# Optimization experiments

Hardware: AMD Instinct MI355X
Metric: run time of the kernel (lower is better)

The kernel has to match this reference:

```python
import jax, jax.numpy as jnp
import numpy as np

N_MSB = 4      # bit planes
WB = 8         # weight quant bits
ABNM = 8       # activation quant bits (non-MVM)
NL = 0.1       # noise level


def quant(x, bits, r):
    # quant_pass: symmetric round-to-grid inside [-r, r]
    s = 2.0 ** (bits - 1)
    xs = jnp.clip(x / r, -1.0 + 1.0 / s, 1.0 - 1.0 / s)
    return jnp.round(xs * s) / s * r


def pact(x, a):
    # pact_a reduces to a hard clip to [-a, a]
    return jnp.clip(x, -a, a)


def bitsplit(x, n_msb):
    # x in [0,1] -> n_msb binary planes y[i] and beta weights l2/l1
    l1 = 2.0 ** n_msb - 1.0
    l2 = 2.0 ** (n_msb - 1 - jnp.arange(n_msb, dtype=x.dtype))  # [n_msb]
    y = jnp.floor(jnp.round(l1 * x)[None] / l2[:, None, None]) % 2.0  # [n_msb,B,D]
    return y, l2 / l1


def noisy_bmm(inp, W, b, key):
    # CustomMM_bmm.forward: quantized weights + additive gaussian noise
    kw, kb = jax.random.split(key)
    nw = jax.lax.stop_gradient(jax.random.normal(kw, W.shape, W.dtype) * W.max() * NL)
    nb = jax.lax.stop_gradient(jax.random.normal(kb, b.shape, b.dtype) * b.max() * NL)
    wq = quant(W, WB, 1.0)
    bq = quant(b, WB, 1.0)
    return jnp.einsum('mbi,mio->mbo', inp, wq + nw) + bq + nb  # [n_msb,B,4H]


def setup_inputs() -> dict:
    key = jax.random.key(0)
    ks = jax.random.split(key, 9)
    B, I, H, M = 4096, 256, 1024, N_MSB
    inp = {
        'input': jax.random.normal(ks[0], (B, I), jnp.float32),
        'hx': jax.random.normal(ks[1], (B, H), jnp.float32),
        'cx': jax.random.normal(ks[2], (B, H), jnp.float32),
        'weight_ih': jax.random.normal(ks[3], (M, I, 4 * H), jnp.float32),
        'weight_hh': jax.random.normal(ks[4], (M, H, 4 * H), jnp.float32),
        'bias_ih': jax.random.normal(ks[5], (M, 1, 4 * H), jnp.float32),
        'bias_hh': jax.random.normal(ks[6], (M, 1, 4 * H), jnp.float32),
        'a1': jnp.array([128.0], jnp.float32),
        'a3': jnp.array([1.0], jnp.float32),
        'a4': jnp.array([1.0], jnp.float32),
        'a5': jnp.array([1.0], jnp.float32),
        'a6': jnp.array([1.0], jnp.float32),
        'a7': jnp.array([4.0], jnp.float32),
        'a8': jnp.array([1.0], jnp.float32),
        'a9': jnp.array([4.0], jnp.float32),
        'a10': jnp.array([1.0], jnp.float32),
        'a11': jnp.array([4.0], jnp.float32),
    }
    return inp


def reference(input, hx, cx, weight_ih, weight_hh, bias_ih, bias_hh,
              a1, a3, a4, a5, a6, a7, a8, a9, a10, a11):
    k1, k2 = jax.random.split(jax.random.key(42))
    # input branch: clip -> map to [0,1] -> bit-split -> noisy bmm -> threshold -> beta-sum
    inp01 = (pact(input, a1) + a1) / (a1 * 2)
    y, beta = bitsplit(inp01, N_MSB)
    out = (noisy_bmm(y, weight_ih, bias_ih, k1) > 0.5).astype(input.dtype)
    part1 = (beta[:, None, None] * out).sum(0) * (a1 * 2) - a1
    # hidden branch (note: '+ a1' offset as in the original source)
    inp01 = (pact(hx, a11) + a1) / (a11 * 2)
    y, beta = bitsplit(inp01, N_MSB)
    out = (noisy_bmm(y, weight_hh, bias_hh, k2) > 0.5).astype(input.dtype)
    part2 = (beta[:, None, None] * out).sum(0) * (a11 * 2) - a11
    gates = part1 + part2  # [B, 4H]
    i, j, f, o = jnp.split(gates, 4, axis=1)
    fg = quant(pact(jax.nn.sigmoid(f), a3), ABNM, a3)
    ig = quant(pact(jax.nn.sigmoid(i), a4), ABNM, a4)
    act = quant(pact(jnp.tanh(j), a5), ABNM, a5)
    og = quant(pact(jax.nn.sigmoid(o), a6), ABNM, a6)
    gated_cell = quant(pact(cx * fg, a7), ABNM, a7)
    activated_input = quant(pact(ig * act, a8), ABNM, a8)
    new_c = quant(pact(gated_cell + activated_input, a9), ABNM, a9)
    activated_cell = quant(pact(jnp.tanh(new_c), a10), ABNM, a10)
    new_h = quant(pact(activated_cell * og, a11), ABNM, a11)
    return new_h, new_c
```

## Files before the change

### kernel.cpp

```cpp
#include <hip/hip_runtime.h>
#include <cstdint>
#include <cstddef>


typedef int v4i __attribute__((ext_vector_type(4)));

struct KPc { uint32_t a, b; };

__host__ __device__ constexpr KPc ctf(uint32_t k0, uint32_t k1v, uint32_t c0, uint32_t c1) {
  uint32_t ks2 = k0 ^ k1v ^ 0x1BD11BDAu;
  uint32_t x0 = c0 + k0;
  uint32_t x1 = c1 + k1v;
  uint32_t r0[4] = {13u, 15u, 26u, 6u};
  uint32_t r1[4] = {17u, 29u, 16u, 24u};
  uint32_t ks[3] = {k0, k1v, ks2};
  for (int g = 0; g < 5; ++g) {
    for (int j = 0; j < 4; ++j) {
      uint32_t rr = (g & 1) ? r1[j] : r0[j];
      x0 += x1;
      x1 = (x1 << rr) | (x1 >> (32u - rr));
      x1 ^= x0;
    }
    x0 += ks[(g + 1) % 3];
    x1 += ks[(g + 2) % 3] + (uint32_t)(g + 1);
  }
  return KPc{x0, x1};
}

constexpr KPc K1K  = ctf(0u, 42u, 0u, 0u);
constexpr KPc K2K  = ctf(0u, 42u, 0u, 1u);
constexpr KPc KWIH = ctf(K1K.a, K1K.b, 0u, 0u);
constexpr KPc KBIH = ctf(K1K.a, K1K.b, 0u, 1u);
constexpr KPc KWHH = ctf(K2K.a, K2K.b, 0u, 0u);
constexpr KPc KBHH = ctf(K2K.a, K2K.b, 0u, 1u);

__device__ __forceinline__ uint32_t tf_bits(uint32_t k0, uint32_t k1v, uint32_t j) {
  KPc r = ctf(k0, k1v, 0u, j);
  return r.a ^ r.b;
}

__device__ __forceinline__ unsigned encf(float f) {
  unsigned u = __float_as_uint(f);
  return (u & 0x80000000u) ? ~u : (u | 0x80000000u);
}
__device__ __forceinline__ float decf(unsigned e) {
  unsigned u = (e & 0x80000000u) ? (e & 0x7FFFFFFFu) : ~e;
  return __uint_as_float(u);
}

__global__ void rmax_kernel(const float* __restrict__ x, int n, unsigned* __restrict__ out) {
  unsigned best = 0u;
  for (int i = blockIdx.x * blockDim.x + threadIdx.x; i < n; i += gridDim.x * blockDim.x) {
    unsigned e = encf(x[i]);
    best = best > e ? best : e;
  }
  for (int off = 32; off > 0; off >>= 1) {
    unsigned o = __shfl_down(best, off, 64);
    best = best > o ? best : o;
  }
  __shared__ unsigned sm[4];
  int lane = threadIdx.x & 63, wv = threadIdx.x >> 6;
  if (lane == 0) sm[wv] = best;
  __syncthreads();
  if (threadIdx.x == 0) {
    unsigned b = sm[0];
    for (int i = 1; i < 4; ++i) b = b > sm[i] ? b : sm[i];
    atomicMax(out, b);
  }
}

__device__ __forceinline__ float xla_log1p(float t) {
  float small = __fmul_rn(__fadd_rn(__fmul_rn(-0.5f, t), 1.0f), t);
  float large = logf(__fadd_rn(t, 1.0f));
  return (fabsf(t) < 1e-4f) ? small : large;
}

__device__ __forceinline__ float xla_erfinv(float x) {
  float w = -xla_log1p(-__fmul_rn(x, x));
  float p;
  if (w < 5.0f) {
    float ww = __fadd_rn(w, -2.5f);
    p = 2.81022636e-08f;
    p = __fadd_rn(3.43273939e-07f, __fmul_rn(p, ww));
    p = __fadd_rn(-3.5233877e-06f, __fmul_rn(p, ww));
    p = __fadd_rn(-4.39150654e-06f, __fmul_rn(p, ww));
    p = __fadd_rn(0.00021858087f, __fmul_rn(p, ww));
    p = __fadd_rn(-0.00125372503f, __fmul_rn(p, ww));
    p = __fadd_rn(-0.00417768164f, __fmul_rn(p, ww));
    p = __fadd_rn(0.246640727f, __fmul_rn(p, ww));
    p = __fadd_rn(1.50140941f, __fmul_rn(p, ww));
  } else {
    float ww = __fadd_rn(sqrtf(w), -3.0f);
    p = -0.000200214257f;
    p = __fadd_rn(0.000100950558f, __fmul_rn(p, ww));
    p = __fadd_rn(0.00134934322f, __fmul_rn(p, ww));
    p = __fadd_rn(-0.00367342844f, __fmul_rn(p, ww));
    p = __fadd_rn(0.00573950773f, __fmul_rn(p, ww));
    p = __fadd_rn(-0.0076224613f, __fmul_rn(p, ww));
    p = __fadd_rn(0.00943887047f, __fmul_rn(p, ww));
    p = __fadd_rn(1.00167406f, __fmul_rn(p, ww));
    p = __fadd_rn(2.83297682f, __fmul_rn(p, ww));
  }
  return __fmul_rn(p, x);
}

__device__ __forceinline__ float normal_from_bits(uint32_t bits) {
  float u01 = __uint_as_float((bits >> 9) | 0x3f800000u) - 1.0f;
  const float lo = -0x1.fffffep-1f;
  float u = fmaxf(lo, __fadd_rn(__fmul_rn(u01, 2.0f), lo));
  return __fmul_rn(0x1.6a09e6p+0f, xla_erfinv(u));
}

__device__ __forceinline__ float quantw(float x) {
  float xs = fminf(fmaxf(x, -0.9921875f), 0.9921875f);
  return __fmul_rn(rintf(__fmul_rn(xs, 128.0f)), 0.0078125f);
}

__global__ void gen_t0_kernel(const float* __restrict__ W, float* __restrict__ T0,
                              const unsigned* __restrict__ encp) {
  int j = blockIdx.x * 256 + threadIdx.x;
  if (j >= 1048576) return;
  float wmax = decf(*encp);
  float nrm = normal_from_bits(tf_bits(KWIH.a, KWIH.b, (uint32_t)j));
  float nw = __fmul_rn(__fmul_rn(nrm, wmax), 0.1f);
  T0[j] = __fadd_rn(quantw(W[j]), nw);
}

__global__ void gen_bias_kernel(const float* __restrict__ bsrc, float* __restrict__ bq,
                                float* __restrict__ nb, int n,
                                const unsigned* __restrict__ encp, uint32_t k0, uint32_t k1v) {
  int j = blockIdx.x * 256 + threadIdx.x;
  if (j >= n) return;
  float bmax = decf(*encp);
  float nrm = normal_from_bits(tf_bits(k0, k1v, (uint32_t)j));
  bq[j] = quantw(bsrc[j]);
  nb[j] = __fmul_rn(__fmul_rn(nrm, bmax), 0.1f);
}

__global__ __launch_bounds__(256) void kv_kernel(
    const float* __restrict__ x, const float* __restrict__ ap,
    const float* __restrict__ offp, unsigned char* __restrict__ kvT, int Kdim) {
  __shared__ unsigned char tile[64][65];
  const int tid = threadIdx.x;
  const int bt = blockIdx.x * 64, it = blockIdx.y * 64;
  const float a = ap[0], off = offp[0];
#pragma unroll
  for (int e = 0; e < 16; ++e) {
    int idx = e * 256 + tid;
    int bl = idx >> 6, il = idx & 63;
    float v = fmaxf(-a, fminf(x[(size_t)(bt + bl) * Kdim + it + il], a));
    float t = __fdiv_rn(__fadd_rn(v, off), __fmul_rn(a, 2.0f));
    int k = (int)rintf(__fmul_rn(15.0f, t));
    tile[il][bl] = (unsigned char)(k & 15);
  }
  __syncthreads();
#pragma unroll
  for (int e = 0; e < 16; ++e) {
    int idx = e * 256 + tid;
    int il = idx >> 6, bl = idx & 63;
    kvT[(size_t)(it + il) * 4096 + bt + bl] = tile[il][bl];
  }
}

__global__ void gen_ahh_kernel(const float* __restrict__ hx, const float* __restrict__ a11p,
                               const float* __restrict__ a1p, signed char* __restrict__ A) {
  int j = blockIdx.x * 256 + threadIdx.x;
  if (j >= 4096 * 1024) return;
  float a = a11p[0], off = a1p[0];
  float v = fmaxf(-a, fminf(hx[j], a));
  float t = __fdiv_rn(__fadd_rn(v, off), __fmul_rn(a, 2.0f));
  int kq = (int)rintf(__fmul_rn(15.0f, t));
  A[j]                      = (signed char)((kq >> 3) & 1);
  A[(size_t)(1 << 22) + j]  = (signed char)((kq >> 2) & 1);
  A[(size_t)(2 << 22) + j]  = (signed char)((kq >> 1) & 1);
  A[(size_t)(3 << 22) + j]  = (signed char)(kq & 1);
}

__global__ void gen_aih_kernel(const float* __restrict__ input, const float* __restrict__ a1p,
                               signed char* __restrict__ A) {
  int j = blockIdx.x * 256 + threadIdx.x;
  if (j >= 4096 * 256) return;
  float a = a1p[0];
  float v = fmaxf(-a, fminf(input[j], a));
  float t = __fdiv_rn(__fadd_rn(v, a), __fmul_rn(a, 2.0f));
  int kq = (int)rintf(__fmul_rn(15.0f, t));
  A[j]                  = (signed char)((kq >> 2) & 1);
  A[1048576 + j]        = (signed char)((kq >> 1) & 1);
  A[2097152 + j]        = (signed char)(kq & 1);
}

__global__ __launch_bounds__(256) void gen_bt_kernel(
    const float* __restrict__ W, signed char* __restrict__ Bt,
    const unsigned* __restrict__ encp, int K, int m0, int nPlanes,
    uint32_t k0k, uint32_t k1k) {
  __shared__ signed char lhi[64 * 68];
  __shared__ signed char llo[64 * 68];
  const int tid = threadIdx.x;
  const int m = m0 + blockIdx.z;
  const int kt = blockIdx.y * 64, ct = blockIdx.x * 64;
  const float wmax = decf(*encp);
#pragma unroll 4
  for (int i = 0; i < 16; ++i) {
    int e = i * 256 + tid;
    int kl = e >> 6, cl = e & 63;
    uint32_t j = (uint32_t)(((m * K + kt + kl) << 12) + ct + cl);
    float nrm = normal_from_bits(tf_bits(k0k, k1k, j));
    float t = __fadd_rn(quantw(W[j]), __fmul_rn(__fmul_rn(nrm, wmax), 0.1f));
    int ti = (int)rintf(__fmul_rn(t, 6144.0f));
    int hi = (ti + 128) >> 8;
    int lo = ti - (hi << 8);
    lhi[cl * 68 + kl] = (signed char)hi;
    llo[cl * 68 + kl] = (signed char)lo;
  }
  __syncthreads();
  const size_t planeElems = (size_t)K << 12;
  signed char* bh = Bt + (size_t)blockIdx.z * planeElems;
  signed char* bl = Bt + (size_t)(nPlanes + blockIdx.z) * planeElems;
#pragma unroll 4
  for (int i = 0; i < 16; ++i) {
    int f = i * 256 + tid;
    int cl = f >> 6, kl = f & 63;
    size_t o = (size_t)(ct + cl) * K + kt + kl;
    bh[o] = lhi[cl * 68 + kl];
    bl[o] = llo[cl * 68 + kl];
  }
}

__global__ __launch_bounds__(256) void gemm_p0_kernel(
    const float* __restrict__ T0, const float* __restrict__ bq, const float* __restrict__ nb,
    const unsigned char* __restrict__ kvT, unsigned char* __restrict__ Kp) {
  const int tid = threadIdx.x, lane = tid & 63, wv = tid >> 6;
  const int c0 = blockIdx.x * 32;
  const int row = blockIdx.y * 256 + wv * 64 + lane;

  float acc[32];
#pragma unroll
  for (int j = 0; j < 32; ++j) acc[j] = 0.0f;

  const unsigned char* kvp = kvT + row;
#pragma unroll 2
  for (int k = 0; k < 256; ++k) {
    unsigned nib = kvp[(size_t)k << 12];
    float f = (float)((nib >> 3) & 1u);
    const float4* tp = (const float4*)(T0 + ((size_t)k << 12) + c0);
    float4 tv[8];
#pragma unroll
    for (int q = 0; q < 8; ++q) tv[q] = tp[q];
#pragma unroll
    for (int q = 0; q < 8; ++q) {
      acc[q * 4 + 0] = __builtin_fmaf(f, tv[q].x, acc[q * 4 + 0]);
      acc[q * 4 + 1] = __builtin_fmaf(f, tv[q].y, acc[q * 4 + 1]);
      acc[q * 4 + 2] = __builtin_fmaf(f, tv[q].z, acc[q * 4 + 2]);
      acc[q * 4 + 3] = __builtin_fmaf(f, tv[q].w, acc[q * 4 + 3]);
    }
  }

#pragma unroll
  for (int j = 0; j < 32; ++j) {
    int col = c0 + j;
    float s = __fadd_rn(__fadd_rn(acc[j], bq[col]), nb[col]);
    Kp[((size_t)row << 12) + col] = (s > 0.5f) ? (unsigned char)8 : (unsigned char)0;
  }
}

typedef __attribute__((address_space(3))) signed char lds_i8;
typedef __attribute__((address_space(1))) const signed char g_i8;

__device__ __forceinline__ void glds16(const signed char* g, signed char* l) {
  __builtin_amdgcn_global_load_lds((g_i8*)g, (lds_i8*)l, 16, 0, 0);
}

__global__ __launch_bounds__(256, 3) void gemm_mfma_kernel(
    const signed char* __restrict__ Ahh, const signed char* __restrict__ Bthh,
    const signed char* __restrict__ Aih, const signed char* __restrict__ Btih,
    const float* __restrict__ bqh, const float* __restrict__ nbh,
    const float* __restrict__ bqi, const float* __restrict__ nbi,
    unsigned char* __restrict__ Kp) {
  const int tid = threadIdx.x;
  const int lane = tid & 63, wv = tid >> 6;
  const int col0 = blockIdx.x * 64;
  const int row0 = blockIdx.y * 128;
  const int wrow = (wv >> 1) * 64;
  const int wcol = (wv & 1) * 32;

  __shared__ __align__(16) signed char smbuf[3][16384];
  const int HOFF = 8192, LOFF = 12288;

  const int l15 = lane & 15;
  const int cc  = (((lane >> 4) ^ ((lane >> 1) & 3)) << 4);
  const int xq  = ((((lane & 3) ^ ((lane >> 3) & 3))) << 4);
  const int lr  = lane >> 2;

  uint32_t k12[4][2];
#pragma unroll
  for (int rf = 0; rf < 4; ++rf) { k12[rf][0] = 0u; k12[rf][1] = 0u; }

  for (int sub = 0; sub < 7; ++sub) {
    int K, w;
    const signed char *A, *Bh, *Bl;
    const float *bqp, *nbp;
    if (sub < 4) {
      int m = sub;
      K = 1024;
      A  = Ahh  + ((size_t)m << 22);
      Bh = Bthh + ((size_t)m << 22);
      Bl = Bthh + ((size_t)(4 + m) << 22);
      bqp = bqh + (m << 12); nbp = nbh + (m << 12);
      w = (1 << (3 - m)) << 4;
    } else {
      int m = sub - 3;
      K = 256;
      A  = Aih  + ((size_t)(m - 1) << 20);
      Bh = Btih + ((size_t)(m - 1) << 20);
      Bl = Btih + ((size_t)(3 + m - 1) << 20);
      bqp = bqi + (m << 12); nbp = nbi + (m << 12);
      w = 1 << (3 - m);
    }

    const size_t soff = (size_t)lr * K + xq;
    const signed char* gA  = A  + (size_t)(row0 + 32 * wv) * K + soff;
    const signed char* gA2 = gA + (size_t)16 * K;
    const signed char* gH  = Bh + (size_t)(col0 + 16 * wv) * K + soff;
    const signed char* gL  = Bl + (size_t)(col0 + 16 * wv) * K + soff;

    auto stage = [&](signed char* base, int k0) {
      glds16(gA  + k0, base + (32 * wv) * 64);
      glds16(gA2 + k0, base + (32 * wv + 16) * 64);
      glds16(gH  + k0, base + HOFF + (16 * wv) * 64);
      glds16(gL  + k0, base + LOFF + (16 * wv) * 64);
    };

    v4i ach[4][2], acl[4][2];
    v4i zero = {0, 0, 0, 0};
#pragma unroll
    for (int rf = 0; rf < 4; ++rf)
#pragma unroll
      for (int cf = 0; cf < 2; ++cf) { ach[rf][cf] = zero; acl[rf][cf] = zero; }

    signed char* bc = &smbuf[0][0];
    signed char* bn = &smbuf[1][0];
    signed char* bf = &smbuf[2][0];

    const int nt = K >> 6;
    stage(bc, 0);
    stage(bn, 64);

    for (int t = 0; t < nt; ++t) {
      if (t + 1 < nt) {
        asm volatile("s_waitcnt vmcnt(4)" ::: "memory");
      } else {
        asm volatile("s_waitcnt vmcnt(0)" ::: "memory");
      }
      __builtin_amdgcn_s_barrier();
      __builtin_amdgcn_sched_barrier(0);
      if (t + 2 < nt) stage(bf, (t + 2) << 6);

      v4i af[4], bfh[2], bfl[2];
#pragma unroll
      for (int rf = 0; rf < 4; ++rf)
        af[rf] = *(const v4i*)(bc + (wrow + rf * 16 + l15) * 64 + cc);
#pragma unroll
      for (int cf = 0; cf < 2; ++cf) {
        bfh[cf] = *(const v4i*)(bc + HOFF + (wcol + cf * 16 + l15) * 64 + cc);
        bfl[cf] = *(const v4i*)(bc + LOFF + (wcol + cf * 16 + l15) * 64 + cc);
      }
#pragma unroll
      for (int rf = 0; rf < 4; ++rf)
#pragma unroll
        for (int cf = 0; cf < 2; ++cf) {
          ach[rf][cf] = __builtin_amdgcn_mfma_i32_16x16x64_i8(af[rf], bfh[cf], ach[rf][cf], 0, 0, 0);
          acl[rf][cf] = __builtin_amdgcn_mfma_i32_16x16x64_i8(af[rf], bfl[cf], acl[rf][cf], 0, 0, 0);
        }
      signed char* tmp = bc; bc = bn; bn = bf; bf = tmp;
    }
    __syncthreads();

#pragma unroll
    for (int cf = 0; cf < 2; ++cf) {
      int col = col0 + wcol + cf * 16 + l15;
      float bqc = bqp[col];
      float nbc = nbp[col];
#pragma unroll
      for (int rf = 0; rf < 4; ++rf)
#pragma unroll
        for (int r = 0; r < 4; ++r) {
          int tot = ach[rf][cf][r] * 256 + acl[rf][cf][r];
          float s = __fmul_rn((float)tot, (1.0f / 6144.0f));
          float s2 = __fadd_rn(__fadd_rn(s, bqc), nbc);
          if (s2 > 0.5f) k12[rf][cf] += ((uint32_t)w << (8 * r));
        }
    }
  }

#pragma unroll
  for (int rf = 0; rf < 4; ++rf)
#pragma unroll
    for (int cf = 0; cf < 2; ++cf)
#pragma unroll
      for (int r = 0; r < 4; ++r) {
        int row = row0 + wrow + rf * 16 + ((lane >> 4) << 2) + r;
        int col = col0 + wcol + cf * 16 + l15;
        size_t o = ((size_t)row << 12) + col;
        Kp[o] = (unsigned char)(Kp[o] | ((k12[rf][cf] >> (8 * r)) & 255u));
      }
}

__device__ __forceinline__ float quant8(float x, float r) {
  float xs = __fdiv_rn(x, r);
  xs = fminf(fmaxf(xs, -0.9921875f), 0.9921875f);
  float q = rintf(__fmul_rn(xs, 128.0f));
  return __fmul_rn(__fdiv_rn(q, 128.0f), r);
}
__device__ __forceinline__ float pactf(float x, float a) { return fminf(fmaxf(x, -a), a); }
__device__ __forceinline__ double sigd(double x) { return 1.0 / (1.0 + exp(-x)); }

__global__ void tail_kernel(const unsigned char* __restrict__ Kp, const float* __restrict__ cx,
                            const float* a1p, const float* a3p, const float* a4p,
                            const float* a5p, const float* a6p, const float* a7p,
                            const float* a8p, const float* a9p, const float* a10p,
                            const float* a11p, float* __restrict__ out) {
  int idx = blockIdx.x * 256 + threadIdx.x;
  if (idx >= 4096 * 1024) return;
  int b = idx >> 10, h = idx & 1023;
  double a1 = (double)a1p[0], a11 = (double)a11p[0];
  const unsigned char* row = Kp + (size_t)b * 4096 + h;
  int pI = row[0], pJ = row[1024], pF = row[2048], pO = row[3072];
  auto gate = [&](int pk) -> double {
    double s1 = (double)(pk & 15) * (1.0 / 15.0);
    double s2 = (double)(pk >> 4) * (1.0 / 15.0);
    return (s1 * (2.0 * a1) - a1) + (s2 * (2.0 * a11) - a11);
  };
  double gi = gate(pI), gj = gate(pJ), gf = gate(pF), go = gate(pO);
  float a3 = a3p[0], a4 = a4p[0], a5 = a5p[0], a6 = a6p[0];
  float a7 = a7p[0], a8 = a8p[0], a9 = a9p[0], a10 = a10p[0], a11f = a11p[0];
  float fg  = quant8(pactf((float)sigd(gf), a3), a3);
  float ig  = quant8(pactf((float)sigd(gi), a4), a4);
  float act = quant8(pactf((float)tanh(gj), a5), a5);
  float og  = quant8(pactf((float)sigd(go), a6), a6);
  float cxv = cx[idx];
  float gc  = quant8(pactf(__fmul_rn(cxv, fg), a7), a7);
  float ai  = quant8(pactf(__fmul_rn(ig, act), a8), a8);
  float nc  = quant8(pactf(__fadd_rn(gc, ai), a9), a9);
  float ac  = quant8(pactf((float)tanh((double)nc), a10), a10);
  float nh  = quant8(pactf(__fmul_rn(ac, og), a11f), a11f);
  out[idx] = nh;
  out[4194304 + idx] = nc;
}

extern "C" void kernel_launch(void* const* d_in, const int* in_sizes, int n_in,
                              void* d_out, int out_size, void* d_ws, size_t ws_size,
                              hipStream_t stream) {
  const float* input = (const float*)d_in[0];
  const float* hx    = (const float*)d_in[1];
  const float* cx    = (const float*)d_in[2];
  const float* wih   = (const float*)d_in[3];
  const float* whh   = (const float*)d_in[4];
  const float* bih   = (const float*)d_in[5];
  const float* bhh   = (const float*)d_in[6];
  const float* a1p   = (const float*)d_in[7];
  const float* a3p   = (const float*)d_in[8];
  const float* a4p   = (const float*)d_in[9];
  const float* a5p   = (const float*)d_in[10];
  const float* a6p   = (const float*)d_in[11];
  const float* a7p   = (const float*)d_in[12];
  const float* a8p   = (const float*)d_in[13];
  const float* a9p   = (const float*)d_in[14];
  const float* a10p  = (const float*)d_in[15];
  const float* a11p  = (const float*)d_in[16];

  char* ws = (char*)d_ws;
  unsigned* enc        = (unsigned*)ws;
  float* T0            = (float*)(ws + 256);
  float* bq_ih         = (float*)(ws + 256 + 4194304);
  float* nb_ih         = bq_ih + 16384;
  float* bq_hh         = nb_ih + 16384;
  float* nb_hh         = bq_hh + 16384;
  unsigned char* kv_ih = (unsigned char*)(nb_hh + 16384);
  signed char* A_hh    = (signed char*)(kv_ih + 1048576);
  signed char* Bt_hh   = A_hh + 16777216;
  signed char* A_ih    = Bt_hh + 33554432;
  signed char* Bt_ih   = A_ih + 3145728;
  unsigned char* Kp    = (unsigned char*)(Bt_ih + 6291456);

  hipMemsetAsync(enc, 0, 64, stream);
  rmax_kernel<<<512, 256, 0, stream>>>(wih, 4 * 256 * 4096, enc + 0);
  rmax_kernel<<<512, 256, 0, stream>>>(whh, 4 * 1024 * 4096, enc + 1);
  rmax_kernel<<<64, 256, 0, stream>>>(bih, 16384, enc + 2);
  rmax_kernel<<<64, 256, 0, stream>>>(bhh, 16384, enc + 3);

  kv_kernel<<<dim3(64, 4), 256, 0, stream>>>(input, a1p, a1p, kv_ih, 256);
  gen_aih_kernel<<<4096, 256, 0, stream>>>(input, a1p, A_ih);
  gen_ahh_kernel<<<16384, 256, 0, stream>>>(hx, a11p, a1p, A_hh);

  gen_bias_kernel<<<64, 256, 0, stream>>>(bih, bq_ih, nb_ih, 16384, enc + 2, KBIH.a, KBIH.b);
  gen_bias_kernel<<<64, 256, 0, stream>>>(bhh, bq_hh, nb_hh, 16384, enc + 3, KBHH.a, KBHH.b);

  gen_t0_kernel<<<4096, 256, 0, stream>>>(wih, T0, enc + 0);
  gen_bt_kernel<<<dim3(64, 16, 4), 256, 0, stream>>>(whh, Bt_hh, enc + 1, 1024, 0, 4,
                                                     KWHH.a, KWHH.b);
  gen_bt_kernel<<<dim3(64, 4, 3), 256, 0, stream>>>(wih, Bt_ih, enc + 0, 256, 1, 3,
                                                    KWIH.a, KWIH.b);

  gemm_p0_kernel<<<dim3(128, 16), 256, 0, stream>>>(T0, bq_ih, nb_ih, kv_ih, Kp);
  gemm_mfma_kernel<<<dim3(64, 32), 256, 0, stream>>>(A_hh, Bt_hh, A_ih, Bt_ih,
                                                     bq_hh, nb_hh, bq_ih, nb_ih, Kp);

  tail_kernel<<<16384, 256, 0, stream>>>(Kp, cx, a1p, a3p, a4p, a5p, a6p, a7p, a8p, a9p,
                                         a10p, a11p, (float*)d_out);
}
```

Measured before the change: 673.6 us.

## Load MFMA B fragments straight to registers and stage p0 T0 in LDS

In the int8 MFMA GEMM, the high and low B-plane fragments are no longer staged through LDS. Each lane loads its 16-byte fragment directly from global memory into registers, one k-tile ahead. This halves the LDS triple-buffer, which now holds only A, and removes the B LDS writes and reads, with the loop unrolled by two to ping-pong the register buffers. Separately, the p0 kernel first copies its 256x32 T0 tile into shared memory so the inner loop reads LDS instead of repeatedly reading global memory. The risks are less coalesced direct global loads for B, extra register pressure, and 32KB of LDS use in p0.

Result: slower. 866.8 us (+28.7%).

```diff
diff --git a/kernel.cpp b/kernel.cpp
--- a/kernel.cpp
+++ b/kernel.cpp
@@ -229,9 +229,17 @@
 __global__ __launch_bounds__(256) void gemm_p0_kernel(
     const float* __restrict__ T0, const float* __restrict__ bq, const float* __restrict__ nb,
     const unsigned char* __restrict__ kvT, unsigned char* __restrict__ Kp) {
+  __shared__ __align__(16) float lt[256 * 32];
   const int tid = threadIdx.x, lane = tid & 63, wv = tid >> 6;
   const int c0 = blockIdx.x * 32;
   const int row = blockIdx.y * 256 + wv * 64 + lane;
+
+#pragma unroll
+  for (int e = 0; e < 32; ++e) {
+    int idx = e * 256 + tid;
+    lt[idx] = T0[((size_t)(idx >> 5) << 12) + c0 + (idx & 31)];
+  }
+  __syncthreads();
 
   float acc[32];
 #pragma unroll
@@ -242,7 +250,7 @@
   for (int k = 0; k < 256; ++k) {
     unsigned nib = kvp[(size_t)k << 12];
     float f = (float)((nib >> 3) & 1u);
-    const float4* tp = (const float4*)(T0 + ((size_t)k << 12) + c0);
+    const float4* tp = (const float4*)(lt + (k << 5));
     float4 tv[8];
 #pragma unroll
     for (int q = 0; q < 8; ++q) tv[q] = tp[q];
@@ -283,13 +291,13 @@
   const int wrow = (wv >> 1) * 64;
   const int wcol = (wv & 1) * 32;
 
-  __shared__ __align__(16) signed char smbuf[3][16384];
-  const int HOFF = 8192, LOFF = 12288;
+  __shared__ __align__(16) signed char smbuf[3][8192];
 
   const int l15 = lane & 15;
   const int cc  = (((lane >> 4) ^ ((lane >> 1) & 3)) << 4);
   const int xq  = ((((lane & 3) ^ ((lane >> 3) & 3))) << 4);
   const int lr  = lane >> 2;
+  const int kch = (lane >> 4) << 4;
 
   uint32_t k12[4][2];
 #pragma unroll
@@ -320,14 +328,12 @@
     const size_t soff = (size_t)lr * K + xq;
     const signed char* gA  = A  + (size_t)(row0 + 32 * wv) * K + soff;
     const signed char* gA2 = gA + (size_t)16 * K;
-    const signed char* gH  = Bh + (size_t)(col0 + 16 * wv) * K + soff;
-    const signed char* gL  = Bl + (size_t)(col0 + 16 * wv) * K + soff;
-
-    auto stage = [&](signed char* base, int k0) {
+    const signed char* pBh = Bh + (size_t)(col0 + wcol + l15) * K + kch;
+    const signed char* pBl = Bl + (size_t)(col0 + wcol + l15) * K + kch;
+
+    auto stageA = [&](signed char* base, int k0) {
       glds16(gA  + k0, base + (32 * wv) * 64);
       glds16(gA2 + k0, base + (32 * wv + 16) * 64);
-      glds16(gH  + k0, base + HOFF + (16 * wv) * 64);
-      glds16(gL  + k0, base + LOFF + (16 * wv) * 64);
     };
 
     v4i ach[4][2], acl[4][2];
@@ -342,36 +348,56 @@
     signed char* bf = &smbuf[2][0];
 
     const int nt = K >> 6;
-    stage(bc, 0);
-    stage(bn, 64);
-
-    for (int t = 0; t < nt; ++t) {
+
+    v4i b0h[2], b0l[2], b1h[2], b1l[2];
+
+    stageA(bc, 0);
+    __builtin_amdgcn_sched_barrier(0);
+#pragma unroll
+    for (int cf = 0; cf < 2; ++cf) {
+      b0h[cf] = *(const v4i*)(pBh + (size_t)cf * 16 * K);
+      b0l[cf] = *(const v4i*)(pBl + (size_t)cf * 16 * K);
+    }
+    __builtin_amdgcn_sched_barrier(0);
+    stageA(bn, 64);
+
+    auto body = [&](int t, v4i (&uh)[2], v4i (&ul)[2], v4i (&lh)[2], v4i (&ll)[2]) {
       if (t + 1 < nt) {
-        asm volatile("s_waitcnt vmcnt(4)" ::: "memory");
+        asm volatile("s_waitcnt vmcnt(2)" ::: "memory");
       } else {
         asm volatile("s_waitcnt vmcnt(0)" ::: "memory");
       }
       __builtin_amdgcn_s_barrier();
       __builtin_amdgcn_sched_barrier(0);
-      if (t + 2 < nt) stage(bf, (t + 2) << 6);
-
-      v4i af[4], bfh[2], bfl[2];
+      if (t + 1 < nt) {
+        int k0 = (t + 1) << 6;
+#pragma unroll
+        for (int cf = 0; cf < 2; ++cf) {
+          lh[cf] = *(const v4i*)(pBh + (size_t)cf * 16 * K + k0);
+          ll[cf] = *(const v4i*)(pBl + (size_t)cf * 16 * K + k0);
+        }
+      }
+      __builtin_amdgcn_sched_barrier(0);
+      if (t + 2 < nt) stageA(bf, (t + 2) << 6);
+      __builtin_amdgcn_sched_barrier(0);
+
+      v4i af[4];
 #pragma unroll
       for (int rf = 0; rf < 4; ++rf)
         af[rf] = *(const v4i*)(bc + (wrow + rf * 16 + l15) * 64 + cc);
 #pragma unroll
-      for (int cf = 0; cf < 2; ++cf) {
-        bfh[cf] = *(const v4i*)(bc + HOFF + (wcol + cf * 16 + l15) * 64 + cc);
-        bfl[cf] = *(const v4i*)(bc + LOFF + (wcol + cf * 16 + l15) * 64 + cc);
-      }
-#pragma unroll
       for (int rf = 0; rf < 4; ++rf)
 #pragma unroll
         for (int cf = 0; cf < 2; ++cf) {
-          ach[rf][cf] = __builtin_amdgcn_mfma_i32_16x16x64_i8(af[rf], bfh[cf], ach[rf][cf], 0, 0, 0);
-          acl[rf][cf] = __builtin_amdgcn_mfma_i32_16x16x64_i8(af[rf], bfl[cf], acl[rf][cf], 0, 0, 0);
+          ach[rf][cf] = __builtin_amdgcn_mfma_i32_16x16x64_i8(af[rf], uh[cf], ach[rf][cf], 0, 0, 0);
+          acl[rf][cf] = __builtin_amdgcn_mfma_i32_16x16x64_i8(af[rf], ul[cf], acl[rf][cf], 0, 0, 0);
         }
       signed char* tmp = bc; bc = bn; bn = bf; bf = tmp;
+    };
+
+    for (int t = 0; t < nt; t += 2) {
+      body(t,     b0h, b0l, b1h, b1l);
+      body(t + 1, b1h, b1l, b0h, b0l);
     }
     __syncthreads();
 
```

## Merge prep launches into two kernels and use lookup tables in tail

Applied to the files above, without the earlier changes.

The four max-reduction launches become a single kernel, and the nine input and weight preparation launches become one large kernel that picks its sub-task from the block index. The tail kernel now builds small shared-memory lookup tables for the gate activations (the inputs are 8-bit codes) and for tanh of the quantized cell. This removes the per-element double-precision exp and tanh, and uses a grid-stride loop with fewer blocks. The aim is to cut launch overhead and tail compute. The cost is divergent branching inside the merged prep kernel and a table-setup step in every tail block.

Result: faster. 582.1 us (-13.6%).

```diff
diff --git a/kernel.cpp b/kernel.cpp
--- a/kernel.cpp
+++ b/kernel.cpp
@@ -48,9 +48,10 @@
   return __uint_as_float(u);
 }
 
-__global__ void rmax_kernel(const float* __restrict__ x, int n, unsigned* __restrict__ out) {
+__device__ __forceinline__ void rmax_seg(const float* __restrict__ x, int n,
+                                         unsigned* __restrict__ out, int rbid, int nblk) {
   unsigned best = 0u;
-  for (int i = blockIdx.x * blockDim.x + threadIdx.x; i < n; i += gridDim.x * blockDim.x) {
+  for (int i = rbid * 256 + threadIdx.x; i < n; i += nblk * 256) {
     unsigned e = encf(x[i]);
     best = best > e ? best : e;
   }
@@ -67,6 +68,16 @@
     for (int i = 1; i < 4; ++i) b = b > sm[i] ? b : sm[i];
     atomicMax(out, b);
   }
+}
+
+__global__ void rmax_all_kernel(const float* __restrict__ wih, const float* __restrict__ whh,
+                                const float* __restrict__ bih, const float* __restrict__ bhh,
+                                unsigned* __restrict__ enc) {
+  int b = blockIdx.x;
+  if (b < 512)       rmax_seg(wih, 4 * 256 * 4096,  enc + 0, b,        512);
+  else if (b < 1024) rmax_seg(whh, 4 * 1024 * 4096, enc + 1, b - 512,  512);
+  else if (b < 1088) rmax_seg(bih, 16384,           enc + 2, b - 1024, 64);
+  else               rmax_seg(bhh, 16384,           enc + 3, b - 1088, 64);
 }
 
 __device__ __forceinline__ float xla_log1p(float t) {
@@ -116,33 +127,12 @@
   return __fmul_rn(rintf(__fmul_rn(xs, 128.0f)), 0.0078125f);
 }
 
-__global__ void gen_t0_kernel(const float* __restrict__ W, float* __restrict__ T0,
-                              const unsigned* __restrict__ encp) {
-  int j = blockIdx.x * 256 + threadIdx.x;
-  if (j >= 1048576) return;
-  float wmax = decf(*encp);
-  float nrm = normal_from_bits(tf_bits(KWIH.a, KWIH.b, (uint32_t)j));
-  float nw = __fmul_rn(__fmul_rn(nrm, wmax), 0.1f);
-  T0[j] = __fadd_rn(quantw(W[j]), nw);
-}
-
-__global__ void gen_bias_kernel(const float* __restrict__ bsrc, float* __restrict__ bq,
-                                float* __restrict__ nb, int n,
-                                const unsigned* __restrict__ encp, uint32_t k0, uint32_t k1v) {
-  int j = blockIdx.x * 256 + threadIdx.x;
-  if (j >= n) return;
-  float bmax = decf(*encp);
-  float nrm = normal_from_bits(tf_bits(k0, k1v, (uint32_t)j));
-  bq[j] = quantw(bsrc[j]);
-  nb[j] = __fmul_rn(__fmul_rn(nrm, bmax), 0.1f);
-}
-
-__global__ __launch_bounds__(256) void kv_kernel(
-    const float* __restrict__ x, const float* __restrict__ ap,
-    const float* __restrict__ offp, unsigned char* __restrict__ kvT, int Kdim) {
-  __shared__ unsigned char tile[64][65];
+__device__ void do_kv(const float* __restrict__ x, const float* __restrict__ ap,
+                      const float* __restrict__ offp, unsigned char* __restrict__ kvT,
+                      int Kdim, int bx, int by, unsigned char* sh) {
+  unsigned char (*tile)[65] = (unsigned char (*)[65])sh;
   const int tid = threadIdx.x;
-  const int bt = blockIdx.x * 64, it = blockIdx.y * 64;
+  const int bt = bx * 64, it = by * 64;
   const float a = ap[0], off = offp[0];
 #pragma unroll
   for (int e = 0; e < 16; ++e) {
@@ -162,9 +152,22 @@
   }
 }
 
-__global__ void gen_ahh_kernel(const float* __restrict__ hx, const float* __restrict__ a11p,
-                               const float* __restrict__ a1p, signed char* __restrict__ A) {
-  int j = blockIdx.x * 256 + threadIdx.x;
+__device__ void do_aih(const float* __restrict__ input, const float* __restrict__ a1p,
+                       signed char* __restrict__ A, int rbid) {
+  int j = rbid * 256 + threadIdx.x;
+  if (j >= 4096 * 256) return;
+  float a = a1p[0];
+  float v = fmaxf(-a, fminf(input[j], a));
+  float t = __fdiv_rn(__fadd_rn(v, a), __fmul_rn(a, 2.0f));
+  int kq = (int)rintf(__fmul_rn(15.0f, t));
+  A[j]                  = (signed char)((kq >> 2) & 1);
+  A[1048576 + j]        = (signed char)((kq >> 1) & 1);
+  A[2097152 + j]        = (signed char)(kq & 1);
+}
+
+__device__ void do_ahh(const float* __restrict__ hx, const float* __restrict__ a11p,
+                       const float* __restrict__ a1p, signed char* __restrict__ A, int rbid) {
+  int j = rbid * 256 + threadIdx.x;
   if (j >= 4096 * 1024) return;
   float a = a11p[0], off = a1p[0];
   float v = fmaxf(-a, fminf(hx[j], a));
@@ -176,28 +179,36 @@
   A[(size_t)(3 << 22) + j]  = (signed char)(kq & 1);
 }
 
-__global__ void gen_aih_kernel(const float* __restrict__ input, const float* __restrict__ a1p,
-                               signed char* __restrict__ A) {
-  int j = blockIdx.x * 256 + threadIdx.x;
-  if (j >= 4096 * 256) return;
-  float a = a1p[0];
-  float v = fmaxf(-a, fminf(input[j], a));
-  float t = __fdiv_rn(__fadd_rn(v, a), __fmul_rn(a, 2.0f));
-  int kq = (int)rintf(__fmul_rn(15.0f, t));
-  A[j]                  = (signed char)((kq >> 2) & 1);
-  A[1048576 + j]        = (signed char)((kq >> 1) & 1);
-  A[2097152 + j]        = (signed char)(kq & 1);
-}
-
-__global__ __launch_bounds__(256) void gen_bt_kernel(
-    const float* __restrict__ W, signed char* __restrict__ Bt,
-    const unsigned* __restrict__ encp, int K, int m0, int nPlanes,
-    uint32_t k0k, uint32_t k1k) {
-  __shared__ signed char lhi[64 * 68];
-  __shared__ signed char llo[64 * 68];
+__device__ void do_bias(const float* __restrict__ bsrc, float* __restrict__ bq,
+                        float* __restrict__ nb, int n, const unsigned* __restrict__ encp,
+                        uint32_t k0, uint32_t k1v, int rbid) {
+  int j = rbid * 256 + threadIdx.x;
+  if (j >= n) return;
+  float bmax = decf(*encp);
+  float nrm = normal_from_bits(tf_bits(k0, k1v, (uint32_t)j));
+  bq[j] = quantw(bsrc[j]);
+  nb[j] = __fmul_rn(__fmul_rn(nrm, bmax), 0.1f);
+}
+
+__device__ void do_t0(const float* __restrict__ W, float* __restrict__ T0,
+                      const unsigned* __restrict__ encp, int rbid) {
+  int j = rbid * 256 + threadIdx.x;
+  if (j >= 1048576) return;
+  float wmax = decf(*encp);
+  float nrm = normal_from_bits(tf_bits(KWIH.a, KWIH.b, (uint32_t)j));
+  float nw = __fmul_rn(__fmul_rn(nrm, wmax), 0.1f);
+  T0[j] = __fadd_rn(quantw(W[j]), nw);
+}
+
+__device__ void do_bt(const float* __restrict__ W, signed char* __restrict__ Bt,
+                      const unsigned* __restrict__ encp, int K, int m0, int nPlanes,
+                      uint32_t k0k, uint32_t k1k, int bx, int by, int bz,
+                      unsigned char* sh) {
+  signed char* lhi = (signed char*)sh;
+  signed char* llo = (signed char*)sh + 4352;
   const int tid = threadIdx.x;
-  const int m = m0 + blockIdx.z;
-  const int kt = blockIdx.y * 64, ct = blockIdx.x * 64;
+  const int m = m0 + bz;
+  const int kt = by * 64, ct = bx * 64;
   const float wmax = decf(*encp);
 #pragma unroll 4
   for (int i = 0; i < 16; ++i) {
@@ -214,8 +225,8 @@
   }
   __syncthreads();
   const size_t planeElems = (size_t)K << 12;
-  signed char* bh = Bt + (size_t)blockIdx.z * planeElems;
-  signed char* bl = Bt + (size_t)(nPlanes + blockIdx.z) * planeElems;
+  signed char* bh = Bt + (size_t)bz * planeElems;
+  signed char* bl = Bt + (size_t)(nPlanes + bz) * planeElems;
 #pragma unroll 4
   for (int i = 0; i < 16; ++i) {
     int f = i * 256 + tid;
@@ -223,6 +234,39 @@
     size_t o = (size_t)(ct + cl) * K + kt + kl;
     bh[o] = lhi[cl * 68 + kl];
     bl[o] = llo[cl * 68 + kl];
+  }
+}
+
+__global__ __launch_bounds__(256) void prep_all_kernel(
+    const float* __restrict__ input, const float* __restrict__ hx,
+    const float* __restrict__ wih, const float* __restrict__ whh,
+    const float* __restrict__ bih, const float* __restrict__ bhh,
+    const float* __restrict__ a1p, const float* __restrict__ a11p,
+    const unsigned* __restrict__ enc,
+    unsigned char* __restrict__ kvT, signed char* __restrict__ A_ih,
+    signed char* __restrict__ A_hh, float* __restrict__ bq_ih, float* __restrict__ nb_ih,
+    float* __restrict__ bq_hh, float* __restrict__ nb_hh, float* __restrict__ T0,
+    signed char* __restrict__ Bt_hh, signed char* __restrict__ Bt_ih) {
+  __shared__ __align__(16) unsigned char sh[8704];
+  int b = blockIdx.x;
+  if (b < 256) {
+    do_kv(input, a1p, a1p, kvT, 256, b & 63, b >> 6, sh);
+  } else if (b < 4352) {
+    do_aih(input, a1p, A_ih, b - 256);
+  } else if (b < 20736) {
+    do_ahh(hx, a11p, a1p, A_hh, b - 4352);
+  } else if (b < 20800) {
+    do_bias(bih, bq_ih, nb_ih, 16384, enc + 2, KBIH.a, KBIH.b, b - 20736);
+  } else if (b < 20864) {
+    do_bias(bhh, bq_hh, nb_hh, 16384, enc + 3, KBHH.a, KBHH.b, b - 20800);
+  } else if (b < 24960) {
+    do_t0(wih, T0, enc + 0, b - 20864);
+  } else if (b < 29056) {
+    int t = b - 24960;
+    do_bt(whh, Bt_hh, enc + 1, 1024, 0, 4, KWHH.a, KWHH.b, t & 63, (t >> 6) & 15, t >> 10, sh);
+  } else {
+    int t = b - 29056;
+    do_bt(wih, Bt_ih, enc + 0, 256, 1, 3, KWIH.a, KWIH.b, t & 63, (t >> 6) & 3, t >> 8, sh);
   }
 }
 
@@ -414,37 +458,55 @@
 __device__ __forceinline__ float pactf(float x, float a) { return fminf(fmaxf(x, -a), a); }
 __device__ __forceinline__ double sigd(double x) { return 1.0 / (1.0 + exp(-x)); }
 
-__global__ void tail_kernel(const unsigned char* __restrict__ Kp, const float* __restrict__ cx,
-                            const float* a1p, const float* a3p, const float* a4p,
-                            const float* a5p, const float* a6p, const float* a7p,
-                            const float* a8p, const float* a9p, const float* a10p,
-                            const float* a11p, float* __restrict__ out) {
-  int idx = blockIdx.x * 256 + threadIdx.x;
-  if (idx >= 4096 * 1024) return;
-  int b = idx >> 10, h = idx & 1023;
-  double a1 = (double)a1p[0], a11 = (double)a11p[0];
-  const unsigned char* row = Kp + (size_t)b * 4096 + h;
-  int pI = row[0], pJ = row[1024], pF = row[2048], pO = row[3072];
-  auto gate = [&](int pk) -> double {
+__global__ __launch_bounds__(256) void tail_kernel(
+    const unsigned char* __restrict__ Kp, const float* __restrict__ cx,
+    const float* a1p, const float* a3p, const float* a4p,
+    const float* a5p, const float* a6p, const float* a7p,
+    const float* a8p, const float* a9p, const float* a10p,
+    const float* a11p, float* __restrict__ out) {
+  __shared__ float Tf[256], Ti[256], Tj[256], To[256], Tac[256];
+  const int tid = threadIdx.x;
+  const double a1 = (double)a1p[0], a11 = (double)a11p[0];
+  const float a3 = a3p[0], a4 = a4p[0], a5 = a5p[0], a6 = a6p[0];
+  const float a7 = a7p[0], a8 = a8p[0], a9 = a9p[0], a10 = a10p[0], a11f = a11p[0];
+
+  {
+    int pk = tid;
     double s1 = (double)(pk & 15) * (1.0 / 15.0);
     double s2 = (double)(pk >> 4) * (1.0 / 15.0);
-    return (s1 * (2.0 * a1) - a1) + (s2 * (2.0 * a11) - a11);
-  };
-  double gi = gate(pI), gj = gate(pJ), gf = gate(pF), go = gate(pO);
-  float a3 = a3p[0], a4 = a4p[0], a5 = a5p[0], a6 = a6p[0];
-  float a7 = a7p[0], a8 = a8p[0], a9 = a9p[0], a10 = a10p[0], a11f = a11p[0];
-  float fg  = quant8(pactf((float)sigd(gf), a3), a3);
-  float ig  = quant8(pactf((float)sigd(gi), a4), a4);
-  float act = quant8(pactf((float)tanh(gj), a5), a5);
-  float og  = quant8(pactf((float)sigd(go), a6), a6);
-  float cxv = cx[idx];
-  float gc  = quant8(pactf(__fmul_rn(cxv, fg), a7), a7);
-  float ai  = quant8(pactf(__fmul_rn(ig, act), a8), a8);
-  float nc  = quant8(pactf(__fadd_rn(gc, ai), a9), a9);
-  float ac  = quant8(pactf((float)tanh((double)nc), a10), a10);
-  float nh  = quant8(pactf(__fmul_rn(ac, og), a11f), a11f);
-  out[idx] = nh;
-  out[4194304 + idx] = nc;
+    double g = (s1 * (2.0 * a1) - a1) + (s2 * (2.0 * a11) - a11);
+    Tf[pk] = quant8(pactf((float)sigd(g), a3), a3);
+    Ti[pk] = quant8(pactf((float)sigd(g), a4), a4);
+    Tj[pk] = quant8(pactf((float)tanh(g), a5), a5);
+    To[pk] = quant8(pactf((float)sigd(g), a6), a6);
+    if (tid < 255) {
+      float qf = (float)(tid - 127);
+      float ncv = __fmul_rn(__fdiv_rn(qf, 128.0f), a9);
+      Tac[tid] = quant8(pactf((float)tanh((double)ncv), a10), a10);
+    }
+  }
+  __syncthreads();
+
+  for (int idx = blockIdx.x * 256 + tid; idx < 4194304; idx += 2048 * 256) {
+    int b = idx >> 10, h = idx & 1023;
+    const unsigned char* row = Kp + (size_t)b * 4096 + h;
+    int pI = row[0], pJ = row[1024], pF = row[2048], pO = row[3072];
+    float fg  = Tf[pF];
+    float ig  = Ti[pI];
+    float act = Tj[pJ];
+    float og  = To[pO];
+    float cxv = cx[idx];
+    float gc  = quant8(pactf(__fmul_rn(cxv, fg), a7), a7);
+    float ai  = quant8(pactf(__fmul_rn(ig, act), a8), a8);
+    float s   = __fadd_rn(gc, ai);
+    float xs  = fminf(fmaxf(__fdiv_rn(pactf(s, a9), a9), -0.9921875f), 0.9921875f);
+    float qf  = rintf(__fmul_rn(xs, 128.0f));
+    float nc  = __fmul_rn(__fdiv_rn(qf, 128.0f), a9);
+    float ac  = Tac[(int)qf + 127];
+    float nh  = quant8(pactf(__fmul_rn(ac, og), a11f), a11f);
+    out[idx] = nh;
+    out[4194304 + idx] = nc;
+  }
 }
 
 extern "C" void kernel_launch(void* const* d_in, const int* in_sizes, int n_in,
@@ -483,28 +545,17 @@
   unsigned char* Kp    = (unsigned char*)(Bt_ih + 6291456);
 
   hipMemsetAsync(enc, 0, 64, stream);
-  rmax_kernel<<<512, 256, 0, stream>>>(wih, 4 * 256 * 4096, enc + 0);
-  rmax_kernel<<<512, 256, 0, stream>>>(whh, 4 * 1024 * 4096, enc + 1);
-  rmax_kernel<<<64, 256, 0, stream>>>(bih, 16384, enc + 2);
-  rmax_kernel<<<64, 256, 0, stream>>>(bhh, 16384, enc + 3);
-
-  kv_kernel<<<dim3(64, 4), 256, 0, stream>>>(input, a1p, a1p, kv_ih, 256);
-  gen_aih_kernel<<<4096, 256, 0, stream>>>(input, a1p, A_ih);
-  gen_ahh_kernel<<<16384, 256, 0, stream>>>(hx, a11p, a1p, A_hh);
-
-  gen_bias_kernel<<<64, 256, 0, stream>>>(bih, bq_ih, nb_ih, 16384, enc + 2, KBIH.a, KBIH.b);
-  gen_bias_kernel<<<64, 256, 0, stream>>>(bhh, bq_hh, nb_hh, 16384, enc + 3, KBHH.a, KBHH.b);
-
-  gen_t0_kernel<<<4096, 256, 0, stream>>>(wih, T0, enc + 0);
-  gen_bt_kernel<<<dim3(64, 16, 4), 256, 0, stream>>>(whh, Bt_hh, enc + 1, 1024, 0, 4,
-                                                     KWHH.a, KWHH.b);
-  gen_bt_kernel<<<dim3(64, 4, 3), 256, 0, stream>>>(wih, Bt_ih, enc + 0, 256, 1, 3,
-                                                    KWIH.a, KWIH.b);
+
+  rmax_all_kernel<<<1152, 256, 0, stream>>>(wih, whh, bih, bhh, enc);
+
+  prep_all_kernel<<<29824, 256, 0, stream>>>(input, hx, wih, whh, bih, bhh, a1p, a11p,
+                                             enc, kv_ih, A_ih, A_hh, bq_ih, nb_ih,
+                                             bq_hh, nb_hh, T0, Bt_hh, Bt_ih);
 
   gemm_p0_kernel<<<dim3(128, 16), 256, 0, stream>>>(T0, bq_ih, nb_ih, kv_ih, Kp);
   gemm_mfma_kernel<<<dim3(64, 32), 256, 0, stream>>>(A_hh, Bt_hh, A_ih, Bt_ih,
                                                      bq_hh, nb_hh, bq_ih, nb_ih, Kp);
 
-  tail_kernel<<<16384, 256, 0, stream>>>(Kp, cx, a1p, a3p, a4p, a5p, a6p, a7p, a8p, a9p,
-                                         a10p, a11p, (float*)d_out);
-}
+  tail_kernel<<<2048, 256, 0, stream>>>(Kp, cx, a1p, a3p, a4p, a5p, a6p, a7p, a8p, a9p,
+                                        a10p, a11p, (float*)d_out);
+}
```
